# Optimization experiments

Measured on AMD Instinct MI355X. Metric: run time of the kernel, lower is better.

## Reference

```python
import jax, jax.numpy as jnp
import numpy as np

H = 64  # LSTM hidden size ('unit' in the torch module)

def _lstm_params(k, scale):
    k1, k2, k3 = jax.random.split(k, 3)
    wih = jax.random.uniform(k1, (4 * H, 1), minval=-scale, maxval=scale, dtype=jnp.float32)
    whh = jax.random.uniform(k2, (4 * H, H), minval=-scale, maxval=scale, dtype=jnp.float32)
    b = jax.random.uniform(k3, (4 * H,), minval=-scale, maxval=scale, dtype=jnp.float32)  # b_ih + b_hh folded
    return wih, whh, b

def _linear_params(k, out_d, in_d):
    k1, k2 = jax.random.split(k)
    s = 1.0 / np.sqrt(in_d)
    w = jax.random.uniform(k1, (out_d, in_d), minval=-s, maxval=s, dtype=jnp.float32)
    b = jax.random.uniform(k2, (out_d,), minval=-s, maxval=s, dtype=jnp.float32)
    return w, b

def setup_inputs():
    key = jax.random.key(0)
    ks = jax.random.split(key, 16)
    B, T, A = 4096, 32, 6
    s = 1.0 / np.sqrt(H)
    inp = {
        'x0': jax.random.normal(ks[0], (B, T, 1), dtype=jnp.float32),
        'x1': jax.random.normal(ks[1], (B, T, 1), dtype=jnp.float32),
        'x2': jax.random.normal(ks[2], (B, T, 1), dtype=jnp.float32),
        's2': jax.random.normal(ks[3], (B, 3), dtype=jnp.float32),
    }
    for name, k in [('q00', ks[4]), ('q01', ks[5]), ('i00', ks[6]), ('i01', ks[7]), ('i02', ks[8])]:
        wih, whh, b = _lstm_params(k, s)
        inp[name + '_wih'], inp[name + '_whh'], inp[name + '_b'] = wih, whh, b
    inp['q03_w'], inp['q03_b'] = _linear_params(ks[9], H, 3)
    inp['q1_w'], inp['q1_b'] = _linear_params(ks[10], H, 4 * H)
    inp['q2_w'], inp['q2_b'] = _linear_params(ks[11], A, H)
    inp['i03_w'], inp['i03_b'] = _linear_params(ks[12], H, 3)
    inp['i1_w'], inp['i1_b'] = _linear_params(ks[13], H, 4 * H)
    inp['i2_w'], inp['i2_b'] = _linear_params(ks[14], A, H)
    return inp

def _lstm_hn(x, wih, whh, b):
    # x: [B,T,1] -> final hidden state h_T: [B,H]. PyTorch gate order: i, f, g, o.
    B = x.shape[0]
    gx = jnp.einsum('bti,gi->btg', x, wih) + b        # [B,T,4H], input part precomputed
    gx = jnp.swapaxes(gx, 0, 1)                        # [T,B,4H]
    h0 = jnp.zeros((B, H), x.dtype)
    def step(carry, g):
        h, c = carry
        g = g + h @ whh.T
        i, f, gg, o = jnp.split(g, 4, axis=-1)
        c = jax.nn.sigmoid(f) * c + jax.nn.sigmoid(i) * jnp.tanh(gg)
        h = jax.nn.sigmoid(o) * jnp.tanh(c)
        return (h, c), None
    (h, _), _ = jax.lax.scan(step, (h0, h0), gx)
    return h

def reference(x0, x1, x2, s2,
              q00_wih, q00_whh, q00_b, q01_wih, q01_whh, q01_b,
              i00_wih, i00_whh, i00_b, i01_wih, i01_whh, i01_b, i02_wih, i02_whh, i02_b,
              q03_w, q03_b, q1_w, q1_b, q2_w, q2_b,
              i03_w, i03_b, i1_w, i1_b, i2_w, i2_b):
    # q branch (NOTE: original code applies q01 to BOTH x1 and x2 -- reproduced faithfully)
    hn0 = _lstm_hn(x0, q00_wih, q00_whh, q00_b)
    hn1 = _lstm_hn(x1, q01_wih, q01_whh, q01_b)
    hn2 = _lstm_hn(x2, q01_wih, q01_whh, q01_b)
    hn3 = jax.nn.relu(s2 @ q03_w.T + q03_b)
    hq = jnp.concatenate([hn0, hn1, hn2, hn3], axis=1)  # [B,4H]
    q = jax.nn.relu(hq @ q1_w.T + q1_b)
    # i branch
    hn0 = _lstm_hn(x0, i00_wih, i00_whh, i00_b)
    hn1 = _lstm_hn(x1, i01_wih, i01_whh, i01_b)
    hn2 = _lstm_hn(x2, i02_wih, i02_whh, i02_b)
    hn3 = jax.nn.relu(s2 @ i03_w.T + i03_b)
    hi = jnp.concatenate([hn0, hn1, hn2, hn3], axis=1)
    i = jax.nn.relu(hi @ i1_w.T + i1_b)
    i = jax.nn.relu(i @ i2_w.T + i2_b)                   # [B,A]
    return (q @ q2_w.T + q2_b, jax.nn.log_softmax(i, axis=1), i)
```

## Files before the change

kernel.cpp:

```cpp
#include <hip/hip_runtime.h>

#define BTOT 4096
#define TS 32

typedef __attribute__((ext_vector_type(8))) short bfrag;
typedef __attribute__((ext_vector_type(4))) float f32x4;

#define S1 (-1.44269504089f)
#define S2 (-2.88539008178f)

__device__ __forceinline__ short f2bf(float f){
  union { float f; unsigned u; } v; v.f = f;
  unsigned r = v.u + 0x7FFFu + ((v.u >> 16) & 1u);
  return (short)(r >> 16);
}
__device__ __forceinline__ float bf2f(short s){
  union { unsigned u; float f; } v; v.u = ((unsigned)(unsigned short)s) << 16; return v.f;
}
__device__ __forceinline__ f32x4 exp2v(f32x4 a){
  f32x4 r;
  r[0] = __builtin_amdgcn_exp2f(a[0]);
  r[1] = __builtin_amdgcn_exp2f(a[1]);
  r[2] = __builtin_amdgcn_exp2f(a[2]);
  r[3] = __builtin_amdgcn_exp2f(a[3]);
  return r;
}
__device__ __forceinline__ f32x4 rcpv(f32x4 a){
  f32x4 r;
  r[0] = __builtin_amdgcn_rcpf(a[0]);
  r[1] = __builtin_amdgcn_rcpf(a[1]);
  r[2] = __builtin_amdgcn_rcpf(a[2]);
  r[3] = __builtin_amdgcn_rcpf(a[3]);
  return r;
}

struct LstmP {
  const float* x[6];
  const float* wih[6];
  const float* whh[6];
  const float* bias[6];
  float* hout;
};

struct EpiP {
  const float* hout;
  const float* s2;
  const float* w03[2]; const float* b03[2];
  const float* w1[2];  const float* b1[2];
  const float* w2[2];  const float* b2[2];
  float* out;
};

__global__ __launch_bounds__(256, 4) void lstm6(LstmP p){
  const int run = blockIdx.y;
  const int b0 = blockIdx.x * 16;
  const int t = threadIdx.x;
  const int w = t >> 6, lane = t & 63;
  const int i16 = lane & 15, q = lane >> 4;

  __shared__ bfrag hb[2][16*9];
  __shared__ float xsT[TS*20];

  const float* __restrict__ whh = p.whh[run];

  bfrag B[4][2];
  float wihv[4], bv[4];
#pragma unroll
  for (int g = 0; g < 4; ++g){
    const float sg = (g == 2) ? S2 : S1;
    const int n = 64*g + 16*w + i16;
    const float* wr = whh + n*64;
#pragma unroll
    for (int kf = 0; kf < 2; ++kf){
      const float* src = wr + 32*kf + 8*q;
      bfrag bb;
#pragma unroll
      for (int j = 0; j < 8; ++j) bb[j] = f2bf(src[j] * sg);
      B[g][kf] = bb;
    }
    wihv[g] = p.wih[run][n] * sg;
    bv[g]   = p.bias[run][n] * sg;
  }
  {
    const float* x = p.x[run] + (size_t)b0 * TS;
    for (int i = t; i < 16*TS; i += 256){
      int m = i & 15, s = i >> 4;
      xsT[s*20 + m] = x[m*TS + s];
    }
    int* hz = (int*)&hb[0][0];
    for (int i = t; i < 576; i += 256) hz[i] = 0;
  }
  __syncthreads();

  f32x4 c4 = {0.f, 0.f, 0.f, 0.f};
  f32x4 hlast;

  for (int s = 0; s < TS; ++s){
    const bfrag* hh = hb[s & 1];
    short* wh = (short*)hb[(s+1) & 1];
    const int af = i16*9 + q;
    bfrag ah0 = hh[af];
    bfrag ah1 = hh[af + 4];
    f32x4 xm4 = *(const f32x4*)(xsT + s*20 + 4*q);

    f32x4 acc[4];
#pragma unroll
    for (int g = 0; g < 4; ++g){
      acc[g] = xm4 * wihv[g] + bv[g];
      acc[g] = __builtin_amdgcn_mfma_f32_16x16x32_bf16(ah0, B[g][0], acc[g], 0,0,0);
      acc[g] = __builtin_amdgcn_mfma_f32_16x16x32_bf16(ah1, B[g][1], acc[g], 0,0,0);
    }
    f32x4 ei = exp2v(acc[0]);
    f32x4 ef = exp2v(acc[1]);
    f32x4 eg = exp2v(acc[2]);
    f32x4 eo = exp2v(acc[3]);
    f32x4 pf = 1.0f + ef;
    f32x4 D1 = (1.0f + eg) * (1.0f + ei);
    f32x4 num = __builtin_elementwise_fma(c4, D1, (1.0f - eg) * pf);
    f32x4 cc = num * rcpv(pf * D1);
    c4 = cc;
    f32x4 ec = exp2v(cc * S2);
    f32x4 hv = (1.0f - ec) * rcpv((1.0f + ec) * (1.0f + eo));
    hlast = hv;
    const int wbase = (4*q)*72 + 16*w + i16;
#pragma unroll
    for (int r = 0; r < 4; ++r)
      wh[wbase + r*72] = f2bf(hv[r]);
    __syncthreads();
  }

#pragma unroll
  for (int r = 0; r < 4; ++r){
    int m = 4*q + r, j = 16*w + i16;
    p.hout[((size_t)run*BTOT + b0 + m)*64 + j] = hlast[r];
  }
}

__global__ __launch_bounds__(256) void epilogue(EpiP p){
  const int br = blockIdx.y;
  const int b0 = blockIdx.x * 16;
  const int t = threadIdx.x;
  const int wave = t >> 6, lane = t & 63;
  const int i16 = lane & 15, q = lane >> 4;

  __shared__ bfrag hqv_hi[16*33], hqv_lo[16*33];
  __shared__ float qv[16*66];
  __shared__ float iv[16][6];

  const float* hbase = p.hout + (size_t)br*3*BTOT*64;
  {
    short4* dh = (short4*)hqv_hi;
    short4* dl = (short4*)hqv_lo;
    for (int i = t; i < 768; i += 256){
      int run = i >> 8, ii = i & 255;
      int e = ii >> 4, j4 = ii & 15;
      float4 v = *(const float4*)(hbase + ((size_t)run*BTOT + b0 + e)*64 + j4*4);
      short4 h, l;
      short x0 = f2bf(v.x); h.x = x0; l.x = f2bf(v.x - bf2f(x0));
      short x1 = f2bf(v.y); h.y = x1; l.y = f2bf(v.y - bf2f(x1));
      short x2 = f2bf(v.z); h.z = x2; l.z = f2bf(v.z - bf2f(x2));
      short x3 = f2bf(v.w); h.w = x3; l.w = f2bf(v.w - bf2f(x3));
      int o4 = e*66 + run*16 + j4;
      dh[o4] = h;
      dl[o4] = l;
    }
  }
  {
    short* sh = (short*)hqv_hi;
    short* sl = (short*)hqv_lo;
    const float* w03 = p.w03[br];
    const float* b03 = p.b03[br];
    for (int i = t; i < 1024; i += 256){
      int e = i >> 6, jj = i & 63;
      const float* s2r = p.s2 + (size_t)(b0 + e)*3;
      float v = fmaf(s2r[0], w03[jj*3+0],
                fmaf(s2r[1], w03[jj*3+1],
                fmaf(s2r[2], w03[jj*3+2], b03[jj])));
      v = fmaxf(v, 0.0f);
      int off = e*264 + 192 + jj;
      short hi = f2bf(v);
      sh[off] = hi;
      sl[off] = f2bf(v - bf2f(hi));
    }
  }
  __syncthreads();

  {
    const int n = 16*wave + i16;
    const float* w1r = p.w1[br] + (size_t)n*256;
    f32x4 acc;
    { float bb = p.b1[br][n]; acc[0]=bb; acc[1]=bb; acc[2]=bb; acc[3]=bb; }
#pragma unroll
    for (int ks = 0; ks < 8; ++ks){
      bfrag ah = hqv_hi[i16*33 + 4*ks + q];
      bfrag al = hqv_lo[i16*33 + 4*ks + q];
      const float* src = w1r + 32*ks + 8*q;
      bfrag bh, bl;
#pragma unroll
      for (int j = 0; j < 8; ++j){
        float f = src[j];
        short hi = f2bf(f);
        bh[j] = hi;
        bl[j] = f2bf(f - bf2f(hi));
      }
      acc = __builtin_amdgcn_mfma_f32_16x16x32_bf16(ah, bh, acc, 0,0,0);
      acc = __builtin_amdgcn_mfma_f32_16x16x32_bf16(al, bh, acc, 0,0,0);
      acc = __builtin_amdgcn_mfma_f32_16x16x32_bf16(ah, bl, acc, 0,0,0);
    }
#pragma unroll
    for (int r = 0; r < 4; ++r)
      qv[(4*q + r)*66 + n] = fmaxf(acc[r], 0.0f);
  }
  __syncthreads();

  if (t < 96){
    int e = t / 6, a = t % 6;
    const float* w2r = p.w2[br] + a*64;
    const float* qe = qv + e*66;
    float acc2 = p.b2[br][a];
#pragma unroll 8
    for (int k = 0; k < 64; ++k) acc2 = fmaf(qe[k], w2r[k], acc2);
    int b = b0 + e;
    if (br == 0){
      p.out[(size_t)b*6 + a] = acc2;
    } else {
      float v = fmaxf(acc2, 0.0f);
      iv[e][a] = v;
      p.out[(size_t)2*BTOT*6 + (size_t)b*6 + a] = v;
    }
  }
  __syncthreads();
  if (br == 1 && t < 16){
    float m = iv[t][0];
    for (int a2 = 1; a2 < 6; ++a2) m = fmaxf(m, iv[t][a2]);
    float ss = 0.0f;
    for (int a2 = 0; a2 < 6; ++a2) ss += __expf(iv[t][a2] - m);
    float ls = __logf(ss);
    int b = b0 + t;
    for (int a2 = 0; a2 < 6; ++a2)
      p.out[(size_t)BTOT*6 + (size_t)b*6 + a2] = iv[t][a2] - m - ls;
  }
}

extern "C" void kernel_launch(void* const* d_in, const int* in_sizes, int n_in,
                              void* d_out, int out_size, void* d_ws, size_t ws_size,
                              hipStream_t stream) {
  const float* x0 = (const float*)d_in[0];
  const float* x1 = (const float*)d_in[1];
  const float* x2 = (const float*)d_in[2];
  const float* s2 = (const float*)d_in[3];

  LstmP lp;
  lp.x[0]=x0; lp.x[1]=x1; lp.x[2]=x2; lp.x[3]=x0; lp.x[4]=x1; lp.x[5]=x2;
  const int wbase[6] = {4, 7, 7, 10, 13, 16};
  for (int r = 0; r < 6; ++r){
    lp.wih[r]  = (const float*)d_in[wbase[r]+0];
    lp.whh[r]  = (const float*)d_in[wbase[r]+1];
    lp.bias[r] = (const float*)d_in[wbase[r]+2];
  }
  lp.hout = (float*)d_ws;

  lstm6<<<dim3(BTOT/16, 6), 256, 0, stream>>>(lp);

  EpiP ep;
  ep.hout = (const float*)d_ws;
  ep.s2 = s2;
  ep.w03[0]=(const float*)d_in[19]; ep.b03[0]=(const float*)d_in[20];
  ep.w1 [0]=(const float*)d_in[21]; ep.b1 [0]=(const float*)d_in[22];
  ep.w2 [0]=(const float*)d_in[23]; ep.b2 [0]=(const float*)d_in[24];
  ep.w03[1]=(const float*)d_in[25]; ep.b03[1]=(const float*)d_in[26];
  ep.w1 [1]=(const float*)d_in[27]; ep.b1 [1]=(const float*)d_in[28];
  ep.w2 [1]=(const float*)d_in[29]; ep.b2 [1]=(const float*)d_in[30];
  ep.out = (float*)d_out;

  epilogue<<<dim3(BTOT/16, 2), 256, 0, stream>>>(ep);
}
```

Measured before the change: 183.0 us.

## Run each LSTM tile in a single wave to remove per-step block barriers

The LSTM kernel now launches one 64-lane wave per 16-row batch tile instead of four waves. That single wave holds all 64 hidden columns' recurrent weights in registers and loops over four column groups at each timestep. This removes the per-step __syncthreads and the initial barrier, and writes the final hidden state to global memory directly on the last step. In exchange, register pressure per wave is much higher and there are four times fewer waves to hide MFMA and transcendental latency.

```diff
diff --git a/kernel.cpp b/kernel.cpp
--- a/kernel.cpp
+++ b/kernel.cpp
@@ -51,11 +51,10 @@
   float* out;
 };
 
-__global__ __launch_bounds__(256, 4) void lstm6(LstmP p){
+__global__ __launch_bounds__(64, 2) void lstm6(LstmP p){
   const int run = blockIdx.y;
   const int b0 = blockIdx.x * 16;
-  const int t = threadIdx.x;
-  const int w = t >> 6, lane = t & 63;
+  const int lane = threadIdx.x;
   const int i16 = lane & 15, q = lane >> 4;
 
   __shared__ bfrag hb[2][16*9];
@@ -63,37 +62,40 @@
 
   const float* __restrict__ whh = p.whh[run];
 
-  bfrag B[4][2];
-  float wihv[4], bv[4];
+  bfrag B[4][4][2];
+  float wihv[4][4], bv[4][4];
 #pragma unroll
   for (int g = 0; g < 4; ++g){
     const float sg = (g == 2) ? S2 : S1;
-    const int n = 64*g + 16*w + i16;
-    const float* wr = whh + n*64;
-#pragma unroll
-    for (int kf = 0; kf < 2; ++kf){
-      const float* src = wr + 32*kf + 8*q;
-      bfrag bb;
-#pragma unroll
-      for (int j = 0; j < 8; ++j) bb[j] = f2bf(src[j] * sg);
-      B[g][kf] = bb;
-    }
-    wihv[g] = p.wih[run][n] * sg;
-    bv[g]   = p.bias[run][n] * sg;
+#pragma unroll
+    for (int cg = 0; cg < 4; ++cg){
+      const int n = 64*g + 16*cg + i16;
+      const float* wr = whh + n*64;
+#pragma unroll
+      for (int kf = 0; kf < 2; ++kf){
+        const float* src = wr + 32*kf + 8*q;
+        bfrag bb;
+#pragma unroll
+        for (int j = 0; j < 8; ++j) bb[j] = f2bf(src[j] * sg);
+        B[g][cg][kf] = bb;
+      }
+      wihv[g][cg] = p.wih[run][n] * sg;
+      bv[g][cg]   = p.bias[run][n] * sg;
+    }
   }
   {
     const float* x = p.x[run] + (size_t)b0 * TS;
-    for (int i = t; i < 16*TS; i += 256){
-      int m = i & 15, s = i >> 4;
-      xsT[s*20 + m] = x[m*TS + s];
+    for (int i = lane; i < 16*TS; i += 64){
+      int m = i >> 5, s = i & 31;
+      xsT[s*20 + m] = x[i];
     }
     int* hz = (int*)&hb[0][0];
-    for (int i = t; i < 576; i += 256) hz[i] = 0;
-  }
-  __syncthreads();
-
-  f32x4 c4 = {0.f, 0.f, 0.f, 0.f};
-  f32x4 hlast;
+    for (int i = lane; i < 576; i += 64) hz[i] = 0;
+  }
+
+  f32x4 c4[4];
+#pragma unroll
+  for (int cg = 0; cg < 4; ++cg) c4[cg] = (f32x4){0.f, 0.f, 0.f, 0.f};
 
   for (int s = 0; s < TS; ++s){
     const bfrag* hh = hb[s & 1];
@@ -103,36 +105,37 @@
     bfrag ah1 = hh[af + 4];
     f32x4 xm4 = *(const f32x4*)(xsT + s*20 + 4*q);
 
-    f32x4 acc[4];
-#pragma unroll
-    for (int g = 0; g < 4; ++g){
-      acc[g] = xm4 * wihv[g] + bv[g];
-      acc[g] = __builtin_amdgcn_mfma_f32_16x16x32_bf16(ah0, B[g][0], acc[g], 0,0,0);
-      acc[g] = __builtin_amdgcn_mfma_f32_16x16x32_bf16(ah1, B[g][1], acc[g], 0,0,0);
-    }
-    f32x4 ei = exp2v(acc[0]);
-    f32x4 ef = exp2v(acc[1]);
-    f32x4 eg = exp2v(acc[2]);
-    f32x4 eo = exp2v(acc[3]);
-    f32x4 pf = 1.0f + ef;
-    f32x4 D1 = (1.0f + eg) * (1.0f + ei);
-    f32x4 num = __builtin_elementwise_fma(c4, D1, (1.0f - eg) * pf);
-    f32x4 cc = num * rcpv(pf * D1);
-    c4 = cc;
-    f32x4 ec = exp2v(cc * S2);
-    f32x4 hv = (1.0f - ec) * rcpv((1.0f + ec) * (1.0f + eo));
-    hlast = hv;
-    const int wbase = (4*q)*72 + 16*w + i16;
-#pragma unroll
-    for (int r = 0; r < 4; ++r)
-      wh[wbase + r*72] = f2bf(hv[r]);
-    __syncthreads();
-  }
-
-#pragma unroll
-  for (int r = 0; r < 4; ++r){
-    int m = 4*q + r, j = 16*w + i16;
-    p.hout[((size_t)run*BTOT + b0 + m)*64 + j] = hlast[r];
+#pragma unroll
+    for (int cg = 0; cg < 4; ++cg){
+      f32x4 acc[4];
+#pragma unroll
+      for (int g = 0; g < 4; ++g){
+        acc[g] = xm4 * wihv[g][cg] + bv[g][cg];
+        acc[g] = __builtin_amdgcn_mfma_f32_16x16x32_bf16(ah0, B[g][cg][0], acc[g], 0,0,0);
+        acc[g] = __builtin_amdgcn_mfma_f32_16x16x32_bf16(ah1, B[g][cg][1], acc[g], 0,0,0);
+      }
+      f32x4 ei = exp2v(acc[0]);
+      f32x4 ef = exp2v(acc[1]);
+      f32x4 eg = exp2v(acc[2]);
+      f32x4 eo = exp2v(acc[3]);
+      f32x4 pf = 1.0f + ef;
+      f32x4 D1 = (1.0f + eg) * (1.0f + ei);
+      f32x4 num = __builtin_elementwise_fma(c4[cg], D1, (1.0f - eg) * pf);
+      f32x4 cc = num * rcpv(pf * D1);
+      c4[cg] = cc;
+      f32x4 ec = exp2v(cc * S2);
+      f32x4 hv = (1.0f - ec) * rcpv((1.0f + ec) * (1.0f + eo));
+      if (s == TS-1){
+#pragma unroll
+        for (int r = 0; r < 4; ++r)
+          p.hout[((size_t)run*BTOT + b0 + 4*q + r)*64 + 16*cg + i16] = hv[r];
+      } else {
+        const int wbase = (4*q)*72 + 16*cg + i16;
+#pragma unroll
+        for (int r = 0; r < 4; ++r)
+          wh[wbase + r*72] = f2bf(hv[r]);
+      }
+    }
   }
 }
 
@@ -260,7 +263,7 @@
   }
   lp.hout = (float*)d_ws;
 
-  lstm6<<<dim3(BTOT/16, 6), 256, 0, stream>>>(lp);
+  lstm6<<<dim3(BTOT/16, 6), 64, 0, stream>>>(lp);
 
   EpiP ep;
   ep.hout = (const float*)d_ws;
```

After: 270.7 us. 48.0% more time.

## Process two 16-row batch tiles per LSTM block to amortize weights and syncs

Applied to the files above, without the earlier changes.

Each LSTM workgroup now handles 32 batch rows as two independent 16-row tiles that share the register-resident recurrent weights and a single barrier per timestep. The grid is halved, so per-block setup (weight loading and bf16 conversion) is amortized over twice the work, and the two tiles give independent MFMA/transcendental chains to interleave. The x staging load is made coalesced, and the final hidden state is written straight from the last step. The cost is fewer blocks (768 versus 1536) with lower occupancy bounds, which may reduce latency hiding across the CUs.

```diff
diff --git a/kernel.cpp b/kernel.cpp
--- a/kernel.cpp
+++ b/kernel.cpp
@@ -51,15 +51,15 @@
   float* out;
 };
 
-__global__ __launch_bounds__(256, 4) void lstm6(LstmP p){
+__global__ __launch_bounds__(256, 3) void lstm6(LstmP p){
   const int run = blockIdx.y;
-  const int b0 = blockIdx.x * 16;
+  const int b0 = blockIdx.x * 32;
   const int t = threadIdx.x;
   const int w = t >> 6, lane = t & 63;
   const int i16 = lane & 15, q = lane >> 4;
 
-  __shared__ bfrag hb[2][16*9];
-  __shared__ float xsT[TS*20];
+  __shared__ bfrag hb[2][2][16*9];
+  __shared__ float xsT[TS*36];
 
   const float* __restrict__ whh = p.whh[run];
 
@@ -83,56 +83,59 @@
   }
   {
     const float* x = p.x[run] + (size_t)b0 * TS;
-    for (int i = t; i < 16*TS; i += 256){
-      int m = i & 15, s = i >> 4;
-      xsT[s*20 + m] = x[m*TS + s];
-    }
-    int* hz = (int*)&hb[0][0];
-    for (int i = t; i < 576; i += 256) hz[i] = 0;
-  }
-  __syncthreads();
-
-  f32x4 c4 = {0.f, 0.f, 0.f, 0.f};
-  f32x4 hlast;
-
+    for (int i = t; i < 32*TS; i += 256){
+      int m = i >> 5, s = i & 31;
+      xsT[s*36 + m] = x[i];
+    }
+    int* hz = (int*)&hb[0][0][0];
+    for (int i = t; i < 1152; i += 256) hz[i] = 0;
+  }
+  __syncthreads();
+
+  f32x4 c4[2];
+  c4[0] = (f32x4){0.f,0.f,0.f,0.f};
+  c4[1] = (f32x4){0.f,0.f,0.f,0.f};
+
+  const int af = i16*9 + q;
   for (int s = 0; s < TS; ++s){
-    const bfrag* hh = hb[s & 1];
-    short* wh = (short*)hb[(s+1) & 1];
-    const int af = i16*9 + q;
-    bfrag ah0 = hh[af];
-    bfrag ah1 = hh[af + 4];
-    f32x4 xm4 = *(const f32x4*)(xsT + s*20 + 4*q);
-
-    f32x4 acc[4];
-#pragma unroll
-    for (int g = 0; g < 4; ++g){
-      acc[g] = xm4 * wihv[g] + bv[g];
-      acc[g] = __builtin_amdgcn_mfma_f32_16x16x32_bf16(ah0, B[g][0], acc[g], 0,0,0);
-      acc[g] = __builtin_amdgcn_mfma_f32_16x16x32_bf16(ah1, B[g][1], acc[g], 0,0,0);
-    }
-    f32x4 ei = exp2v(acc[0]);
-    f32x4 ef = exp2v(acc[1]);
-    f32x4 eg = exp2v(acc[2]);
-    f32x4 eo = exp2v(acc[3]);
-    f32x4 pf = 1.0f + ef;
-    f32x4 D1 = (1.0f + eg) * (1.0f + ei);
-    f32x4 num = __builtin_elementwise_fma(c4, D1, (1.0f - eg) * pf);
-    f32x4 cc = num * rcpv(pf * D1);
-    c4 = cc;
-    f32x4 ec = exp2v(cc * S2);
-    f32x4 hv = (1.0f - ec) * rcpv((1.0f + ec) * (1.0f + eo));
-    hlast = hv;
-    const int wbase = (4*q)*72 + 16*w + i16;
-#pragma unroll
-    for (int r = 0; r < 4; ++r)
-      wh[wbase + r*72] = f2bf(hv[r]);
+#pragma unroll
+    for (int tile = 0; tile < 2; ++tile){
+      const bfrag* hh = hb[s & 1][tile];
+      short* wh = (short*)hb[(s+1) & 1][tile];
+      bfrag ah0 = hh[af];
+      bfrag ah1 = hh[af + 4];
+      f32x4 xm4 = *(const f32x4*)(xsT + s*36 + 16*tile + 4*q);
+
+      f32x4 acc[4];
+#pragma unroll
+      for (int g = 0; g < 4; ++g){
+        acc[g] = xm4 * wihv[g] + bv[g];
+        acc[g] = __builtin_amdgcn_mfma_f32_16x16x32_bf16(ah0, B[g][0], acc[g], 0,0,0);
+        acc[g] = __builtin_amdgcn_mfma_f32_16x16x32_bf16(ah1, B[g][1], acc[g], 0,0,0);
+      }
+      f32x4 ei = exp2v(acc[0]);
+      f32x4 ef = exp2v(acc[1]);
+      f32x4 eg = exp2v(acc[2]);
+      f32x4 eo = exp2v(acc[3]);
+      f32x4 pf = 1.0f + ef;
+      f32x4 D1 = (1.0f + eg) * (1.0f + ei);
+      f32x4 num = __builtin_elementwise_fma(c4[tile], D1, (1.0f - eg) * pf);
+      f32x4 cc = num * rcpv(pf * D1);
+      c4[tile] = cc;
+      f32x4 ec = exp2v(cc * S2);
+      f32x4 hv = (1.0f - ec) * rcpv((1.0f + ec) * (1.0f + eo));
+      if (s == TS-1){
+#pragma unroll
+        for (int r = 0; r < 4; ++r)
+          p.hout[((size_t)run*BTOT + b0 + 16*tile + 4*q + r)*64 + 16*w + i16] = hv[r];
+      } else {
+        const int wbase = (4*q)*72 + 16*w + i16;
+#pragma unroll
+        for (int r = 0; r < 4; ++r)
+          wh[wbase + r*72] = f2bf(hv[r]);
+      }
+    }
     __syncthreads();
-  }
-
-#pragma unroll
-  for (int r = 0; r < 4; ++r){
-    int m = 4*q + r, j = 16*w + i16;
-    p.hout[((size_t)run*BTOT + b0 + m)*64 + j] = hlast[r];
   }
 }
 
@@ -260,7 +263,7 @@
   }
   lp.hout = (float*)d_ws;
 
-  lstm6<<<dim3(BTOT/16, 6), 256, 0, stream>>>(lp);
+  lstm6<<<dim3(BTOT/32, 6), 256, 0, stream>>>(lp);
 
   EpiP ep;
   ep.hout = (const float*)d_ws;
```

After: 184.5 us. About the same (+0.8%).
